# Optimization experiments

Measured on AMD Instinct MI355X. Metric: run time of the kernel, lower is better.

The kernel has to match this reference:

```python
import jax, jax.numpy as jnp
import numpy as np

B, T, D = 4, 2048, 2048
H, HD = 16, 128          # heads, head_dim (H*HD == D)
I = 5632                 # intermediate size
CAP = 0.25
K = int(T * CAP)         # 512 tokens selected per batch row
S = B * K                # packed sequence length
THETA = 10000.0
EPS = 1e-6


def setup_inputs() -> dict:
    key = jax.random.key(0)
    ks = jax.random.split(key, 12)
    s = 0.02
    w = lambda k, shp: jax.random.normal(k, shp, jnp.float32) * s
    return {
        "hidden_states": jax.random.normal(ks[0], (B, T, D), jnp.float32),
        "router_w": w(ks[1], (D,)),
        "router_b": jnp.zeros((1,), jnp.float32),
        "ln1_w": jnp.ones((D,), jnp.float32),
        "ln2_w": jnp.ones((D,), jnp.float32),
        "wq": w(ks[2], (D, D)), "bq": jnp.zeros((D,), jnp.float32),
        "wk": w(ks[3], (D, D)), "bk": jnp.zeros((D,), jnp.float32),
        "wv": w(ks[4], (D, D)), "bv": jnp.zeros((D,), jnp.float32),
        "wo": w(ks[5], (D, D)),
        "w_gate": w(ks[6], (D, I)),
        "w_up": w(ks[7], (D, I)),
        "w_down": w(ks[8], (I, D)),
    }


def _rms(x, w):
    return x * jax.lax.rsqrt(jnp.mean(x * x, axis=-1, keepdims=True) + EPS) * w


def _rotate_half(x):
    x1, x2 = jnp.split(x, 2, axis=-1)
    return jnp.concatenate([-x2, x1], axis=-1)


def reference(hidden_states, router_w, router_b, ln1_w, ln2_w,
              wq, bq, wk, bk, wv, bv, wo, w_gate, w_up, w_down):
    # ---- router: per-token scalar scores, top-k per batch row ----
    scores = hidden_states @ router_w + router_b[0]          # [B,T]
    _, idx = jax.lax.top_k(scores, K)                        # [B,K]
    idx = jnp.sort(idx, axis=-1)                             # causal order in packed seq

    # ---- gather selected tokens into packed batch-1 sequence ----
    sel = jnp.take_along_axis(hidden_states, idx[..., None], axis=1)  # [B,K,D]
    sel_scores = jnp.take_along_axis(scores, idx, axis=1)             # [B,K]
    x = sel.reshape(S, D)
    pos = idx.reshape(S)                                     # original token positions

    # ---- rotary tables gathered at original positions ----
    inv_freq = 1.0 / (THETA ** (jnp.arange(0, HD, 2, dtype=jnp.float32) / HD))
    freqs = pos.astype(jnp.float32)[:, None] * inv_freq[None, :]      # [S,HD/2]
    emb = jnp.concatenate([freqs, freqs], axis=-1)                    # [S,HD]
    cos, sin = jnp.cos(emb)[:, None, :], jnp.sin(emb)[:, None, :]     # [S,1,HD]

    # ---- Qwen2 decoder block (attention) ----
    h = _rms(x, ln1_w)
    q = (h @ wq + bq).reshape(S, H, HD)
    k = (h @ wk + bk).reshape(S, H, HD)
    v = (h @ wv + bv).reshape(S, H, HD)
    q = q * cos + _rotate_half(q) * sin
    k = k * cos + _rotate_half(k) * sin

    att = jnp.einsum("shd,thd->hst", q, k) / np.sqrt(HD).astype(np.float32)
    causal = jnp.tril(jnp.ones((S, S), bool))
    att = jnp.where(causal[None], att, jnp.finfo(att.dtype).min)
    p = jax.nn.softmax(att, axis=-1)
    attn_out = jnp.einsum("hst,thd->shd", p, v).reshape(S, D) @ wo
    x1 = x + attn_out

    # ---- Qwen2 decoder block (SwiGLU MLP) ----
    h2 = _rms(x1, ln2_w)
    mlp = (jax.nn.silu(h2 @ w_gate) * (h2 @ w_up)) @ w_down
    processed = x1 + mlp                                     # [S,D]

    # ---- sigmoid gate blend + scatter back ----
    gate = jax.nn.sigmoid(sel_scores).reshape(S, 1)
    blended = gate * processed + (1.0 - gate) * x            # [S,D]
    out = hidden_states.at[jnp.arange(B)[:, None], idx].set(blended.reshape(B, K, D))
    return out
```

## Files before the change

kernel.cpp:

```cpp
#include <hip/hip_runtime.h>
#include <stdint.h>

#define B_ 4
#define T_ 2048
#define D_ 2048
#define H_ 16
#define HD_ 128
#define I_ 5632
#define K_ 512
#define S_ 2048
#define D3_ (3 * D_)

typedef float f32x4 __attribute__((ext_vector_type(4)));
typedef short s16x8 __attribute__((ext_vector_type(8)));
typedef __bf16 bf16x8 __attribute__((ext_vector_type(8)));

template <typename V>
__device__ __forceinline__ auto mfma_try(V a, V b, f32x4 c, int)
    -> decltype(__builtin_amdgcn_mfma_f32_16x16x32_bf16(a, b, c, 0, 0, 0)) {
  return __builtin_amdgcn_mfma_f32_16x16x32_bf16(a, b, c, 0, 0, 0);
}
template <typename V>
__device__ __forceinline__ f32x4 mfma_try(V a, V b, f32x4 c, long) {
  return __builtin_amdgcn_mfma_f32_16x16x32_bf16(
      __builtin_bit_cast(bf16x8, a), __builtin_bit_cast(bf16x8, b), c, 0, 0, 0);
}
__device__ __forceinline__ f32x4 mfma_bf16(s16x8 a, s16x8 b, f32x4 c) {
  return mfma_try(a, b, c, 0);
}

__device__ __forceinline__ void gl_lds16(const void* g, void* l) {
  __builtin_amdgcn_global_load_lds((const __attribute__((address_space(1))) void*)g,
                                   (__attribute__((address_space(3))) void*)l, 16, 0, 0);
}

__device__ __forceinline__ unsigned short f2bf(float f) {
  unsigned u = __float_as_uint(f);
  u += 0x7FFFu + ((u >> 16) & 1);
  return (unsigned short)(u >> 16);
}
__device__ __forceinline__ float bf2f(unsigned short s) {
  return __uint_as_float(((unsigned)s) << 16);
}

__global__ __launch_bounds__(256) void k_copy_scores(const float4* __restrict__ hid,
                                                     float4* __restrict__ dst,
                                                     const float4* __restrict__ rw,
                                                     const float* __restrict__ rb,
                                                     float* __restrict__ scores) {
  int row = blockIdx.x, t = threadIdx.x;
  const float4* hr = hid + (size_t)row * (D_ / 4);
  float4* dr = dst + (size_t)row * (D_ / 4);
  float acc = 0.f;
#pragma unroll
  for (int i = 0; i < 2; i++) {
    float4 v = hr[t + i * 256];
    dr[t + i * 256] = v;
    float4 w = rw[t + i * 256];
    acc += v.x * w.x + v.y * w.y + v.z * w.z + v.w * w.w;
  }
#pragma unroll
  for (int d = 32; d; d >>= 1) acc += __shfl_xor(acc, d);
  __shared__ float red[4];
  if ((t & 63) == 0) red[t >> 6] = acc;
  __syncthreads();
  if (t == 0) scores[row] = red[0] + red[1] + red[2] + red[3] + rb[0];
}

__global__ __launch_bounds__(1024) void k_topk(const float* __restrict__ scores,
                                               int* __restrict__ pos) {
  __shared__ unsigned long long keys[T_];
  __shared__ int sidx[K_];
  int b = blockIdx.x, t = threadIdx.x;
  for (int i = t; i < T_; i += 1024) {
    unsigned u = __float_as_uint(scores[b * T_ + i]);
    u = (u & 0x80000000u) ? ~u : (u | 0x80000000u);
    keys[i] = ((unsigned long long)u << 32) | (unsigned)(~(unsigned)i);
  }
  __syncthreads();
  for (int k = 2; k <= T_; k <<= 1)
    for (int j = k >> 1; j > 0; j >>= 1) {
      for (int i = t; i < T_; i += 1024) {
        int l = i ^ j;
        if (l > i) {
          unsigned long long a = keys[i], c = keys[l];
          bool desc = ((i & k) == 0);
          if (desc ? (a < c) : (a > c)) { keys[i] = c; keys[l] = a; }
        }
      }
      __syncthreads();
    }
  if (t < K_) sidx[t] = (int)(~(unsigned)(keys[t] & 0xFFFFFFFFull));
  __syncthreads();
  for (int k = 2; k <= K_; k <<= 1)
    for (int j = k >> 1; j > 0; j >>= 1) {
      if (t < K_) {
        int i = t, l = i ^ j;
        if (l > i && l < K_) {
          int a = sidx[i], c = sidx[l];
          bool asc = ((i & k) == 0);
          if (asc ? (a > c) : (a < c)) { sidx[i] = c; sidx[l] = a; }
        }
      }
      __syncthreads();
    }
  if (t < K_) pos[b * K_ + t] = sidx[t];
}

__global__ __launch_bounds__(256) void k_gather(const float* __restrict__ hidden,
    const int* __restrict__ pos, const float* __restrict__ scores,
    const float* __restrict__ ln1w, float* __restrict__ x,
    unsigned short* __restrict__ xn, float* __restrict__ gate,
    float* __restrict__ cosb, float* __restrict__ sinb) {
  int s = blockIdx.x, t = threadIdx.x;
  int b = s >> 9, p = pos[s];
  const float* src = hidden + ((size_t)b * T_ + p) * D_;
  float v[8];
  float ss = 0.f;
#pragma unroll
  for (int i = 0; i < 8; i++) { v[i] = src[t + i * 256]; ss += v[i] * v[i]; }
  __shared__ float red[4];
#pragma unroll
  for (int d = 32; d; d >>= 1) ss += __shfl_xor(ss, d);
  if ((t & 63) == 0) red[t >> 6] = ss;
  __syncthreads();
  ss = red[0] + red[1] + red[2] + red[3];
  float scale = rsqrtf(ss / (float)D_ + 1e-6f);
  float* xd = x + (size_t)s * D_;
  unsigned short* xnd = xn + (size_t)s * D_;
#pragma unroll
  for (int i = 0; i < 8; i++) {
    int c = t + i * 256;
    xd[c] = v[i];
    xnd[c] = f2bf(v[i] * scale * ln1w[c]);
  }
  if (t == 0) gate[s] = 1.f / (1.f + expf(-scores[b * T_ + p]));
  if (t < 64) {
    float invf = powf(10000.0f, -(float)t / 64.0f);
    float f = (float)p * invf;
    cosb[s * 64 + t] = cosf(f);
    sinb[s * 64 + t] = sinf(f);
  }
}

__global__ __launch_bounds__(256) void k_transpose(const float* __restrict__ src,
                                                   unsigned short* __restrict__ dst,
                                                   int R, int C) {
  __shared__ float tile[32][33];
  int tx = threadIdx.x & 31, ty = threadIdx.x >> 5;
  int c0 = blockIdx.x * 32, r0 = blockIdx.y * 32;
#pragma unroll
  for (int i = 0; i < 4; i++) {
    int r = ty + i * 8;
    tile[r][tx] = src[(size_t)(r0 + r) * C + c0 + tx];
  }
  __syncthreads();
  int drow = threadIdx.x >> 3;
  int dc4 = (threadIdx.x & 7) * 4;
  ushort4 v;
  v.x = f2bf(tile[dc4 + 0][drow]);
  v.y = f2bf(tile[dc4 + 1][drow]);
  v.z = f2bf(tile[dc4 + 2][drow]);
  v.w = f2bf(tile[dc4 + 3][drow]);
  *(ushort4*)&dst[(size_t)(c0 + drow) * R + r0 + dc4] = v;
}

#define SWZ(row) ((((row) >> 1) & 3) << 4)

__device__ __forceinline__ void stage16k(const unsigned short* __restrict__ g, int ldK,
                                         int row0, int k0, char* lds, int tid) {
#pragma unroll
  for (int c = 0; c < 2; c++) {
    int off = c * 8192 + tid * 16;
    int row = off >> 6;
    int cb = (off & 63) ^ SWZ(row);
    gl_lds16(g + (size_t)(row0 + row) * ldK + k0 + (cb >> 1), lds + off);
  }
}
__device__ __forceinline__ void stage8k(const unsigned short* __restrict__ g, int ldK,
                                        int row0, int k0, char* lds, int tid) {
  int off = tid * 16;
  int row = off >> 6;
  int cb = (off & 63) ^ SWZ(row);
  gl_lds16(g + (size_t)(row0 + row) * ldK + k0 + (cb >> 1), lds + off);
}
__device__ __forceinline__ void stage64r(const unsigned short* __restrict__ g, int ldK,
                                         int row0, int k0, char* lds, int tid) {
  int off = tid * 16;
  int row = off >> 6;
  int cb = (off & 63) ^ SWZ(row);
  gl_lds16(g + (size_t)(row0 + row) * ldK + k0 + (cb >> 1), lds + off);
}
__device__ __forceinline__ void stage128r(const unsigned short* __restrict__ g, int ldK,
                                          int row0, int k0, char* lds, int tid) {
#pragma unroll
  for (int c = 0; c < 2; c++) {
    int off = c * 4096 + tid * 16;
    int row = off >> 6;
    int cb = (off & 63) ^ SWZ(row);
    gl_lds16(g + (size_t)(row0 + row) * ldK + k0 + (cb >> 1), lds + off);
  }
}
__device__ __forceinline__ s16x8 ldfrag(const char* base, int row, int g) {
  return *(const s16x8*)(base + row * 64 + ((g * 16) ^ SWZ(row)));
}

__global__ __launch_bounds__(512, 2) void k_gemm_qkv8(const unsigned short* __restrict__ A,
    const unsigned short* __restrict__ Bt, unsigned short* __restrict__ C,
    const float* __restrict__ bq, const float* __restrict__ bk,
    const float* __restrict__ bv) {
  alignas(16) __shared__ short As[2][256 * 32];
  alignas(16) __shared__ short Bs[2][128 * 32];
  int tid = threadIdx.x;
  int lane = tid & 63, g = lane >> 4, lr = lane & 15;
  int wid = tid >> 6, wm = wid >> 1, wn = wid & 1;
  int m0 = blockIdx.x * 256, n0 = blockIdx.y * 128;
  f32x4 zero4 = {0.f, 0.f, 0.f, 0.f};
  f32x4 acc[4][4];
#pragma unroll
  for (int m = 0; m < 4; m++)
#pragma unroll
    for (int n = 0; n < 4; n++) acc[m][n] = zero4;
  const int nkt = D_ / 32;
  stage16k(A, D_, m0, 0, (char*)As[0], tid);
  stage8k(Bt, D_, n0, 0, (char*)Bs[0], tid);
  stage16k(A, D_, m0, 32, (char*)As[1], tid);
  stage8k(Bt, D_, n0, 32, (char*)Bs[1], tid);
  int arow = wm * 64 + lr;
  int brow = wn * 64 + lr;
  for (int t = 0; t < nkt; t++) {
    int b = t & 1;
    const char* Ab = (const char*)As[b];
    const char* Bb = (const char*)Bs[b];
    if (t + 1 < nkt) asm volatile("s_waitcnt vmcnt(3)" ::: "memory");
    else             asm volatile("s_waitcnt vmcnt(0)" ::: "memory");
    __builtin_amdgcn_s_barrier();
    s16x8 af[4], bf4[4];
#pragma unroll
    for (int i = 0; i < 4; i++) af[i] = ldfrag(Ab, arow + i * 16, g);
#pragma unroll
    for (int i = 0; i < 4; i++) bf4[i] = ldfrag(Bb, brow + i * 16, g);
    asm volatile("s_waitcnt lgkmcnt(0)" ::: "memory");
    __builtin_amdgcn_s_barrier();
    if (t + 2 < nkt) {
      stage16k(A, D_, m0, (t + 2) * 32, (char*)As[b], tid);
      stage8k(Bt, D_, n0, (t + 2) * 32, (char*)Bs[b], tid);
    }
    __builtin_amdgcn_s_setprio(1);
#pragma unroll
    for (int m = 0; m < 4; m++)
#pragma unroll
      for (int n = 0; n < 4; n++) acc[m][n] = mfma_bf16(af[m], bf4[n], acc[m][n]);
    __builtin_amdgcn_s_setprio(0);
  }
#pragma unroll
  for (int m = 0; m < 4; m++)
#pragma unroll
    for (int n = 0; n < 4; n++)
#pragma unroll
      for (int r = 0; r < 4; r++) {
        int row = m0 + wm * 64 + m * 16 + (g << 2) + r;
        int col = n0 + wn * 64 + n * 16 + lr;
        float bias = (col < D_) ? bq[col] : ((col < 2 * D_) ? bk[col - D_] : bv[col - 2 * D_]);
        C[(size_t)row * D3_ + col] = f2bf(acc[m][n][r] + bias);
      }
}

__device__ __forceinline__ void stage_u(const unsigned short* __restrict__ g, int ldK,
                                        int grow0, int k0, char* ldsbase, int tid) {
#pragma unroll
  for (int c = 0; c < 2; c++) {
    int off = c * 8192 + tid * 16;
    int row = off >> 7;
    int cb = (off & 127) ^ ((row & 7) << 4);
    gl_lds16(g + (size_t)(grow0 + row) * ldK + k0 + (cb >> 1), ldsbase + off);
  }
}
__device__ __forceinline__ s16x8 ldfrag128(const char* base, int row, int byteoff) {
  return *(const s16x8*)(base + row * 128 + (byteoff ^ ((row & 7) << 4)));
}

#define GUP_MFMA(AF, BB, ACC)                                       \
  __builtin_amdgcn_s_barrier();                                     \
  asm volatile("s_waitcnt lgkmcnt(0)" ::: "memory");                \
  __builtin_amdgcn_sched_barrier(0);                                \
  __builtin_amdgcn_s_setprio(1);                                    \
  _Pragma("unroll") for (int m = 0; m < 4; m++)                     \
    _Pragma("unroll") for (int n = 0; n < 4; n++)                   \
      ACC[m][n] = mfma_bf16(AF[m], BB[n], ACC[m][n]);               \
  __builtin_amdgcn_s_setprio(0);                                    \
  __builtin_amdgcn_s_barrier();

__global__ __launch_bounds__(512, 1) void k_gemm_gup8p(const unsigned short* __restrict__ A,
    const unsigned short* __restrict__ Bg, const unsigned short* __restrict__ Bu,
    unsigned short* __restrict__ act) {
  alignas(16) __shared__ char L[2][65536];
  int tid = threadIdx.x;
  int lane = tid & 63, g = lane >> 4, lr = lane & 15;
  int wid = tid >> 6, wm = wid >> 1, wn = wid & 1;
  int m0 = blockIdx.x * 256, n0 = blockIdx.y * 128;
  f32x4 zero4 = {0.f, 0.f, 0.f, 0.f};
  f32x4 ag[4][4], au[4][4];
#pragma unroll
  for (int m = 0; m < 4; m++)
#pragma unroll
    for (int n = 0; n < 4; n++) { ag[m][n] = zero4; au[m][n] = zero4; }
  int arow = wm * 64 + lr;
  int brow = wn * 64 + lr;
  const int NI = D_ / 128;
  stage_u(A, D_, m0, 0, &L[0][0], tid);
  stage_u(A, D_, m0 + 128, 0, &L[0][16384], tid);
  stage_u(Bg, D_, n0, 0, &L[0][32768], tid);
  stage_u(Bu, D_, n0, 0, &L[0][49152], tid);
  stage_u(A, D_, m0, 64, &L[1][0], tid);
  asm volatile("s_waitcnt vmcnt(2)" ::: "memory");
  __builtin_amdgcn_s_barrier();
  for (int i = 0; i < NI; i++) {
    const char* B0 = &L[0][0];
    const char* B1 = &L[1][0];
    int k1 = i * 128 + 64;
    int k2 = i * 128 + 128;
    int k3 = i * 128 + 192;
    bool more = (i + 1 < NI);
    s16x8 af0[4], af1[4], bb[4];
#pragma unroll
    for (int q = 0; q < 4; q++) af0[q] = ldfrag128(B0, arow + q * 16, g * 16);
#pragma unroll
    for (int q = 0; q < 4; q++) bb[q] = ldfrag128(B0 + 32768, brow + q * 16, g * 16);
    stage_u(A, D_, m0 + 128, k1, &L[1][16384], tid);
    asm volatile("s_waitcnt vmcnt(4)" ::: "memory");
    GUP_MFMA(af0, bb, ag);
#pragma unroll
    for (int q = 0; q < 4; q++) bb[q] = ldfrag128(B0 + 49152, brow + q * 16, g * 16);
    stage_u(Bg, D_, n0, k1, &L[1][32768], tid);
    GUP_MFMA(af0, bb, au);
#pragma unroll
    for (int q = 0; q < 4; q++) af1[q] = ldfrag128(B0, arow + q * 16, 64 + g * 16);
#pragma unroll
    for (int q = 0; q < 4; q++) bb[q] = ldfrag128(B0 + 32768, brow + q * 16, 64 + g * 16);
    stage_u(Bu, D_, n0, k1, &L[1][49152], tid);
    GUP_MFMA(af1, bb, ag);
#pragma unroll
    for (int q = 0; q < 4; q++) bb[q] = ldfrag128(B0 + 49152, brow + q * 16, 64 + g * 16);
    if (more) {
      stage_u(A, D_, m0, k2, &L[0][0], tid);
      asm volatile("s_waitcnt vmcnt(4)" ::: "memory");
    } else {
      asm volatile("s_waitcnt vmcnt(0)" ::: "memory");
    }
    GUP_MFMA(af1, bb, au);
#pragma unroll
    for (int q = 0; q < 4; q++) af0[q] = ldfrag128(B1, arow + q * 16, g * 16);
#pragma unroll
    for (int q = 0; q < 4; q++) bb[q] = ldfrag128(B1 + 32768, brow + q * 16, g * 16);
    if (more) stage_u(A, D_, m0 + 128, k2, &L[0][16384], tid);
    asm volatile("s_waitcnt vmcnt(4)" ::: "memory");
    GUP_MFMA(af0, bb, ag);
#pragma unroll
    for (int q = 0; q < 4; q++) bb[q] = ldfrag128(B1 + 49152, brow + q * 16, g * 16);
    if (more) stage_u(Bg, D_, n0, k2, &L[0][32768], tid);
    GUP_MFMA(af0, bb, au);
#pragma unroll
    for (int q = 0; q < 4; q++) af1[q] = ldfrag128(B1, arow + q * 16, 64 + g * 16);
#pragma unroll
    for (int q = 0; q < 4; q++) bb[q] = ldfrag128(B1 + 32768, brow + q * 16, 64 + g * 16);
    if (more) stage_u(Bu, D_, n0, k2, &L[0][49152], tid);
    GUP_MFMA(af1, bb, ag);
#pragma unroll
    for (int q = 0; q < 4; q++) bb[q] = ldfrag128(B1 + 49152, brow + q * 16, 64 + g * 16);
    if (more) stage_u(A, D_, m0, k3, &L[1][0], tid);
    asm volatile("s_waitcnt vmcnt(4)" ::: "memory");
    GUP_MFMA(af1, bb, au);
  }
#pragma unroll
  for (int m = 0; m < 4; m++)
#pragma unroll
    for (int n = 0; n < 4; n++)
#pragma unroll
      for (int r = 0; r < 4; r++) {
        int row = m0 + wm * 64 + m * 16 + (g << 2) + r;
        int col = n0 + wn * 64 + n * 16 + lr;
        float gv = ag[m][n][r], uv = au[m][n][r];
        float si = gv / (1.f + __expf(-gv));
        act[(size_t)row * I_ + col] = f2bf(si * uv);
      }
}

__global__ __launch_bounds__(256, 2) void k_gemm_wo64(const unsigned short* __restrict__ A,
    const unsigned short* __restrict__ Bt, const float* __restrict__ xres,
    float* __restrict__ x1) {
  alignas(16) __shared__ short As[2][64 * 32];
  alignas(16) __shared__ short Bs[2][128 * 32];
  int tid = threadIdx.x;
  int lane = tid & 63, g = lane >> 4, lr = lane & 15, wid = tid >> 6;
  int m0 = blockIdx.x * 64, n0 = blockIdx.y * 128;
  f32x4 zero4 = {0.f, 0.f, 0.f, 0.f};
  f32x4 acc[4][2];
#pragma unroll
  for (int m = 0; m < 4; m++)
#pragma unroll
    for (int n = 0; n < 2; n++) acc[m][n] = zero4;
  const int nkt = D_ / 32;
  stage64r(A, D_, m0, 0, (char*)As[0], tid);
  stage128r(Bt, D_, n0, 0, (char*)Bs[0], tid);
  stage64r(A, D_, m0, 32, (char*)As[1], tid);
  stage128r(Bt, D_, n0, 32, (char*)Bs[1], tid);
  for (int t = 0; t < nkt; t++) {
    int b = t & 1;
    const char* Ab = (const char*)As[b];
    const char* Bb = (const char*)Bs[b];
    if (t + 1 < nkt) asm volatile("s_waitcnt vmcnt(3)" ::: "memory");
    else             asm volatile("s_waitcnt vmcnt(0)" ::: "memory");
    __builtin_amdgcn_s_barrier();
    s16x8 af[4], bf2[2];
#pragma unroll
    for (int i = 0; i < 4; i++) af[i] = ldfrag(Ab, i * 16 + lr, g);
#pragma unroll
    for (int j = 0; j < 2; j++) bf2[j] = ldfrag(Bb, wid * 32 + j * 16 + lr, g);
    asm volatile("s_waitcnt lgkmcnt(0)" ::: "memory");
    __builtin_amdgcn_s_barrier();
    if (t + 2 < nkt) {
      stage64r(A, D_, m0, (t + 2) * 32, (char*)As[b], tid);
      stage128r(Bt, D_, n0, (t + 2) * 32, (char*)Bs[b], tid);
    }
    __builtin_amdgcn_s_setprio(1);
#pragma unroll
    for (int m = 0; m < 4; m++)
#pragma unroll
      for (int n = 0; n < 2; n++) acc[m][n] = mfma_bf16(af[m], bf2[n], acc[m][n]);
    __builtin_amdgcn_s_setprio(0);
  }
#pragma unroll
  for (int m = 0; m < 4; m++)
#pragma unroll
    for (int n = 0; n < 2; n++)
#pragma unroll
      for (int r = 0; r < 4; r++) {
        int row = m0 + m * 16 + (g << 2) + r;
        int col = n0 + wid * 32 + n * 16 + lr;
        x1[(size_t)row * D_ + col] = acc[m][n][r] + xres[(size_t)row * D_ + col];
      }
}

__global__ __launch_bounds__(256, 2) void k_gemm_down64(const unsigned short* __restrict__ A,
    const unsigned short* __restrict__ Bt, const float* __restrict__ x1,
    const float* __restrict__ x, const float* __restrict__ gate,
    const int* __restrict__ pos, float* __restrict__ out) {
  alignas(16) __shared__ short As[2][64 * 32];
  alignas(16) __shared__ short Bs[2][128 * 32];
  int tid = threadIdx.x;
  int lane = tid & 63, g = lane >> 4, lr = lane & 15, wid = tid >> 6;
  int m0 = blockIdx.x * 64, n0 = blockIdx.y * 128;
  f32x4 zero4 = {0.f, 0.f, 0.f, 0.f};
  f32x4 acc[4][2];
#pragma unroll
  for (int m = 0; m < 4; m++)
#pragma unroll
    for (int n = 0; n < 2; n++) acc[m][n] = zero4;
  const int nkt = I_ / 32;
  stage64r(A, I_, m0, 0, (char*)As[0], tid);
  stage128r(Bt, I_, n0, 0, (char*)Bs[0], tid);
  stage64r(A, I_, m0, 32, (char*)As[1], tid);
  stage128r(Bt, I_, n0, 32, (char*)Bs[1], tid);
  for (int t = 0; t < nkt; t++) {
    int b = t & 1;
    const char* Ab = (const char*)As[b];
    const char* Bb = (const char*)Bs[b];
    if (t + 1 < nkt) asm volatile("s_waitcnt vmcnt(3)" ::: "memory");
    else             asm volatile("s_waitcnt vmcnt(0)" ::: "memory");
    __builtin_amdgcn_s_barrier();
    s16x8 af[4], bf2[2];
#pragma unroll
    for (int i = 0; i < 4; i++) af[i] = ldfrag(Ab, i * 16 + lr, g);
#pragma unroll
    for (int j = 0; j < 2; j++) bf2[j] = ldfrag(Bb, wid * 32 + j * 16 + lr, g);
    asm volatile("s_waitcnt lgkmcnt(0)" ::: "memory");
    __builtin_amdgcn_s_barrier();
    if (t + 2 < nkt) {
      stage64r(A, I_, m0, (t + 2) * 32, (char*)As[b], tid);
      stage128r(Bt, I_, n0, (t + 2) * 32, (char*)Bs[b], tid);
    }
    __builtin_amdgcn_s_setprio(1);
#pragma unroll
    for (int m = 0; m < 4; m++)
#pragma unroll
      for (int n = 0; n < 2; n++) acc[m][n] = mfma_bf16(af[m], bf2[n], acc[m][n]);
    __builtin_amdgcn_s_setprio(0);
  }
#pragma unroll
  for (int m = 0; m < 4; m++)
#pragma unroll
    for (int n = 0; n < 2; n++)
#pragma unroll
      for (int r = 0; r < 4; r++) {
        int srow = m0 + m * 16 + (g << 2) + r;
        int col = n0 + wid * 32 + n * 16 + lr;
        float proc = acc[m][n][r] + x1[(size_t)srow * D_ + col];
        float gt = gate[srow];
        float xv = x[(size_t)srow * D_ + col];
        int bb = srow >> 9;
        int p = pos[srow];
        out[((size_t)bb * T_ + p) * D_ + col] = gt * proc + (1.f - gt) * xv;
      }
}

__global__ __launch_bounds__(256) void k_rope(const unsigned short* __restrict__ qkv,
    const float* __restrict__ cosb, const float* __restrict__ sinb,
    unsigned short* __restrict__ qh, unsigned short* __restrict__ kh,
    unsigned short* __restrict__ vT) {
  int s0 = blockIdx.x * 64;
  int h = blockIdx.y;
  int t = threadIdx.x;
#pragma unroll
  for (int i = 0; i < 16; i++) {
    int flat = t + i * 256;
    int r = flat >> 6, dp = flat & 63;
    int s = s0 + r;
    float c = cosb[s * 64 + dp], sn = sinb[s * 64 + dp];
    const unsigned short* qrow = qkv + (size_t)s * D3_ + h * HD_;
    float q1 = bf2f(qrow[dp]), q2 = bf2f(qrow[dp + 64]);
    unsigned short* qdst = qh + ((size_t)h * S_ + s) * HD_;
    qdst[dp] = f2bf(q1 * c - q2 * sn);
    qdst[dp + 64] = f2bf(q2 * c + q1 * sn);
    const unsigned short* krow = qrow + D_;
    float k1 = bf2f(krow[dp]), k2 = bf2f(krow[dp + 64]);
    unsigned short* kdst = kh + ((size_t)h * S_ + s) * HD_;
    kdst[dp] = f2bf(k1 * c - k2 * sn);
    kdst[dp + 64] = f2bf(k2 * c + k1 * sn);
  }
  __shared__ unsigned short vt[128][66];
#pragma unroll
  for (int i = 0; i < 32; i++) {
    int flat = t + i * 256;
    int r = flat >> 7, d = flat & 127;
    vt[d][r] = qkv[(size_t)(s0 + r) * D3_ + 2 * D_ + h * HD_ + d];
  }
  __syncthreads();
#pragma unroll
  for (int i = 0; i < 32; i++) {
    int flat = t + i * 256;
    int d = flat >> 6, sc = flat & 63;
    vT[((size_t)h * HD_ + d) * S_ + s0 + sc] = vt[d][sc];
  }
}

__device__ __forceinline__ void stage_kv(const unsigned short* __restrict__ kh,
                                         const unsigned short* __restrict__ vT,
                                         size_t hbase, int kt, char* KsB, char* VsB, int tid) {
#pragma unroll
  for (int c = 0; c < 4; c++) {
    int off = c * 4096 + tid * 16;
    int row = off >> 8;
    int cb = (off & 255) ^ ((row & 7) << 4);
    gl_lds16(kh + hbase + (size_t)(kt * 64 + row) * HD_ + (cb >> 1), KsB + off);
  }
#pragma unroll
  for (int c = 0; c < 4; c++) {
    int off = c * 4096 + tid * 16;
    int row = off >> 7;
    int cb = (off & 127) ^ ((row & 7) << 4);
    gl_lds16(vT + hbase + (size_t)row * S_ + kt * 64 + (cb >> 1), VsB + off);
  }
}

__global__ __launch_bounds__(256, 2) void k_attn(const unsigned short* __restrict__ qh,
                                                 const unsigned short* __restrict__ kh,
                                                 const unsigned short* __restrict__ vT,
                                                 unsigned short* __restrict__ ao) {
  alignas(16) __shared__ short Ks[2][64 * 128];
  alignas(16) __shared__ short Vs[2][128 * 64];
  alignas(16) __shared__ short Ps[4][16 * 64];
  int bidx = blockIdx.x;
  int head = bidx & 15;
  int slot = bidx >> 4;
  int qt = (slot < 16) ? (31 - slot) : (slot - 16);
  int q0 = qt * 64;
  int tid = threadIdx.x, w = tid >> 6, lane = tid & 63, g = lane >> 4, lr = lane & 15;
  size_t hbase = (size_t)head * S_ * HD_;
  int qw = q0 + w * 16;
  char* PsW = (char*)&Ps[w][0];
  s16x8 qf[4];
#pragma unroll
  for (int ks = 0; ks < 4; ks++)
    qf[ks] = *(const s16x8*)&qh[hbase + (size_t)(qw + lr) * HD_ + ks * 32 + g * 8];
  f32x4 o[8];
  f32x4 zero4 = {0.f, 0.f, 0.f, 0.f};
#pragma unroll
  for (int nf = 0; nf < 8; nf++) o[nf] = zero4;
  float m_i[4], l_i[4];
#pragma unroll
  for (int r = 0; r < 4; r++) { m_i[r] = -1e30f; l_i[r] = 0.f; }
  const float sc = 0.08838834764831843f;

  stage_kv(kh, vT, hbase, 0, (char*)Ks[0], (char*)Vs[0], tid);
  if (qt > 0) stage_kv(kh, vT, hbase, 1, (char*)Ks[1], (char*)Vs[1], tid);

  for (int kt = 0; kt <= qt; kt++) {
    int b = kt & 1;
    const char* KsB = (const char*)Ks[b];
    const char* VsB = (const char*)Vs[b];
    if (kt < qt) asm volatile("s_waitcnt vmcnt(8)" ::: "memory");
    else         asm volatile("s_waitcnt vmcnt(0)" ::: "memory");
    __builtin_amdgcn_s_barrier();
    f32x4 sacc[4];
#pragma unroll
    for (int nf = 0; nf < 4; nf++) sacc[nf] = zero4;
#pragma unroll
    for (int ks = 0; ks < 4; ks++) {
      s16x8 kf[4];
#pragma unroll
      for (int nf = 0; nf < 4; nf++) {
        int row = nf * 16 + lr;
        kf[nf] = *(const s16x8*)(KsB + row * 256 + (((ks << 6) + (g << 4)) ^ ((row & 7) << 4)));
      }
#pragma unroll
      for (int nf = 0; nf < 4; nf++) sacc[nf] = mfma_bf16(qf[ks], kf[nf], sacc[nf]);
    }
    bool diag = (kt == qt);
#pragma unroll
    for (int r = 0; r < 4; r++) {
      int prow = (g << 2) + r;
      int qrow = qw + prow;
      float pv[4];
      float mx = -1e30f;
#pragma unroll
      for (int nf = 0; nf < 4; nf++) {
        float vv = sacc[nf][r] * sc;
        if (diag) {
          int kc = kt * 64 + nf * 16 + lr;
          vv = (kc <= qrow) ? vv : -1e30f;
        }
        pv[nf] = vv;
        mx = fmaxf(mx, vv);
      }
#pragma unroll
      for (int d = 1; d < 16; d <<= 1) mx = fmaxf(mx, __shfl_xor(mx, d));
      float mold = m_i[r], mnew = fmaxf(mold, mx);
      float corr = __expf(mold - mnew);
      float ssum = 0.f;
#pragma unroll
      for (int nf = 0; nf < 4; nf++) {
        float pe = __expf(pv[nf] - mnew);
        int cb = ((nf * 16 + lr) << 1) ^ ((prow & 7) << 4);
        *(unsigned short*)(PsW + prow * 128 + cb) = f2bf(pe);
        ssum += pe;
      }
#pragma unroll
      for (int d = 1; d < 16; d <<= 1) ssum += __shfl_xor(ssum, d);
      l_i[r] = l_i[r] * corr + ssum;
      m_i[r] = mnew;
#pragma unroll
      for (int nf = 0; nf < 8; nf++) o[nf][r] *= corr;
    }
    s16x8 pa[2];
#pragma unroll
    for (int ks = 0; ks < 2; ks++)
      pa[ks] = *(const s16x8*)(PsW + lr * 128 + (((ks << 6) + (g << 4)) ^ ((lr & 7) << 4)));
#pragma unroll
    for (int nf = 0; nf < 8; nf++) {
#pragma unroll
      for (int ks = 0; ks < 2; ks++) {
        int row = nf * 16 + lr;
        s16x8 vb = *(const s16x8*)(VsB + row * 128 + (((ks << 6) + (g << 4)) ^ ((row & 7) << 4)));
        o[nf] = mfma_bf16(pa[ks], vb, o[nf]);
      }
    }
    asm volatile("s_waitcnt lgkmcnt(0)" ::: "memory");
    __builtin_amdgcn_s_barrier();
    if (kt + 2 <= qt)
      stage_kv(kh, vT, hbase, kt + 2, (char*)Ks[b], (char*)Vs[b], tid);
  }
#pragma unroll
  for (int nf = 0; nf < 8; nf++)
#pragma unroll
    for (int r = 0; r < 4; r++) {
      int row = qw + (g << 2) + r;
      int col = head * HD_ + nf * 16 + lr;
      ao[(size_t)row * D_ + col] = f2bf(o[nf][r] / l_i[r]);
    }
}

__global__ __launch_bounds__(256) void k_rms2(const float* __restrict__ x1,
                                              const float* __restrict__ ln2w,
                                              unsigned short* __restrict__ xn2) {
  int s = blockIdx.x, t = threadIdx.x;
  const float* src = x1 + (size_t)s * D_;
  float v[8];
  float ss = 0.f;
#pragma unroll
  for (int i = 0; i < 8; i++) { v[i] = src[t + i * 256]; ss += v[i] * v[i]; }
  __shared__ float red[4];
#pragma unroll
  for (int d = 32; d; d >>= 1) ss += __shfl_xor(ss, d);
  if ((t & 63) == 0) red[t >> 6] = ss;
  __syncthreads();
  ss = red[0] + red[1] + red[2] + red[3];
  float scale = rsqrtf(ss / (float)D_ + 1e-6f);
  unsigned short* dst = xn2 + (size_t)s * D_;
#pragma unroll
  for (int i = 0; i < 8; i++) {
    int c = t + i * 256;
    dst[c] = f2bf(v[i] * scale * ln2w[c]);
  }
}

extern "C" void kernel_launch(void* const* d_in, const int* in_sizes, int n_in,
                              void* d_out, int out_size, void* d_ws, size_t ws_size,
                              hipStream_t stream) {
  (void)in_sizes; (void)n_in; (void)out_size; (void)ws_size;
  const float* hidden = (const float*)d_in[0];
  const float* router_w = (const float*)d_in[1];
  const float* router_b = (const float*)d_in[2];
  const float* ln1w = (const float*)d_in[3];
  const float* ln2w = (const float*)d_in[4];
  const float* wq = (const float*)d_in[5];
  const float* bq = (const float*)d_in[6];
  const float* wk = (const float*)d_in[7];
  const float* bk = (const float*)d_in[8];
  const float* wv = (const float*)d_in[9];
  const float* bv = (const float*)d_in[10];
  const float* wo = (const float*)d_in[11];
  const float* wg = (const float*)d_in[12];
  const float* wu = (const float*)d_in[13];
  const float* wd = (const float*)d_in[14];
  float* out = (float*)d_out;

  char* ws = (char*)d_ws;
  size_t off = 0;
  auto alloc = [&](size_t bytes) {
    char* p = ws + off;
    off += (bytes + 255) & ~(size_t)255;
    return p;
  };
  unsigned short* wqkvT = (unsigned short*)alloc(3ull * D_ * D_ * 2);
  unsigned short* woT = (unsigned short*)alloc((size_t)D_ * D_ * 2);
  unsigned short* wgT = (unsigned short*)alloc((size_t)I_ * D_ * 2);
  unsigned short* wuT = (unsigned short*)alloc((size_t)I_ * D_ * 2);
  unsigned short* wdT = (unsigned short*)alloc((size_t)D_ * I_ * 2);
  float* scores = (float*)alloc((size_t)B_ * T_ * 4);
  int* pos = (int*)alloc((size_t)S_ * 4);
  float* gate = (float*)alloc((size_t)S_ * 4);
  float* x = (float*)alloc((size_t)S_ * D_ * 4);
  float* x1 = (float*)alloc((size_t)S_ * D_ * 4);
  unsigned short* xn = (unsigned short*)alloc((size_t)S_ * D_ * 2);
  float* cosb = (float*)alloc((size_t)S_ * 64 * 4);
  float* sinb = (float*)alloc((size_t)S_ * 64 * 4);
  unsigned short* qkv = (unsigned short*)alloc((size_t)S_ * D3_ * 2);
  unsigned short* qh = (unsigned short*)alloc((size_t)H_ * S_ * HD_ * 2);
  unsigned short* kh = (unsigned short*)alloc((size_t)H_ * S_ * HD_ * 2);
  unsigned short* vT = (unsigned short*)alloc((size_t)H_ * S_ * HD_ * 2);
  unsigned short* ao = (unsigned short*)alloc((size_t)S_ * D_ * 2);

  k_copy_scores<<<B_ * T_, 256, 0, stream>>>((const float4*)hidden, (float4*)out,
                                             (const float4*)router_w, router_b, scores);

  k_transpose<<<dim3(D_ / 32, D_ / 32), 256, 0, stream>>>(wq, wqkvT, D_, D_);
  k_transpose<<<dim3(D_ / 32, D_ / 32), 256, 0, stream>>>(wk, wqkvT + (size_t)D_ * D_, D_, D_);
  k_transpose<<<dim3(D_ / 32, D_ / 32), 256, 0, stream>>>(wv, wqkvT + 2ull * D_ * D_, D_, D_);
  k_transpose<<<dim3(D_ / 32, D_ / 32), 256, 0, stream>>>(wo, woT, D_, D_);
  k_transpose<<<dim3(I_ / 32, D_ / 32), 256, 0, stream>>>(wg, wgT, D_, I_);
  k_transpose<<<dim3(I_ / 32, D_ / 32), 256, 0, stream>>>(wu, wuT, D_, I_);
  k_transpose<<<dim3(D_ / 32, I_ / 32), 256, 0, stream>>>(wd, wdT, I_, D_);

  k_topk<<<B_, 1024, 0, stream>>>(scores, pos);
  k_gather<<<S_, 256, 0, stream>>>(hidden, pos, scores, ln1w, x, xn, gate, cosb, sinb);

  k_gemm_qkv8<<<dim3(S_ / 256, D3_ / 128), 512, 0, stream>>>(xn, wqkvT, qkv, bq, bk, bv);
  k_rope<<<dim3(S_ / 64, H_), 256, 0, stream>>>(qkv, cosb, sinb, qh, kh, vT);
  k_attn<<<32 * H_, 256, 0, stream>>>(qh, kh, vT, ao);
  k_gemm_wo64<<<dim3(S_ / 64, D_ / 128), 256, 0, stream>>>(ao, woT, x, x1);
  k_rms2<<<S_, 256, 0, stream>>>(x1, ln2w, xn);
  k_gemm_gup8p<<<dim3(S_ / 256, I_ / 128), 512, 0, stream>>>(xn, wgT, wuT, qkv);
  k_gemm_down64<<<dim3(S_ / 64, D_ / 128), 256, 0, stream>>>(qkv, wdT, x1, x, gate, pos, out);
}
```

Baseline: 537.5 us.

## Use 256x256 ping-pong QKV GEMM and batch weight transposes into fewer launches

Replaces the 256x128 double-buffered QKV GEMM with a 256x256 tile kernel using 128-wide K stages, a 64KB-per-buffer LDS ping-pong and phased MFMA blocks interleaved with async global-to-LDS loads, modeled on the gate/up kernel. The larger tile raises arithmetic intensity per byte loaded, and the phased schedule aims to overlap loads with compute. The trade-off is one block per CU, fewer blocks (192), and more accumulator registers. Separately, the weight transposes are merged into two batched launches via blockIdx.z to cut launch overhead.

```diff
diff --git a/kernel.cpp b/kernel.cpp
--- a/kernel.cpp
+++ b/kernel.cpp
@@ -143,9 +143,9 @@
   }
 }
 
-__global__ __launch_bounds__(256) void k_transpose(const float* __restrict__ src,
-                                                   unsigned short* __restrict__ dst,
-                                                   int R, int C) {
+__device__ __forceinline__ void transpose_body(const float* __restrict__ src,
+                                               unsigned short* __restrict__ dst,
+                                               int R, int C) {
   __shared__ float tile[32][33];
   int tx = threadIdx.x & 31, ty = threadIdx.x >> 5;
   int c0 = blockIdx.x * 32, r0 = blockIdx.y * 32;
@@ -164,26 +164,30 @@
   v.w = f2bf(tile[dc4 + 3][drow]);
   *(ushort4*)&dst[(size_t)(c0 + drow) * R + r0 + dc4] = v;
 }
+__global__ __launch_bounds__(256) void k_transpose(const float* __restrict__ src,
+                                                   unsigned short* __restrict__ dst,
+                                                   int R, int C) {
+  transpose_body(src, dst, R, C);
+}
+__global__ __launch_bounds__(256) void k_transpose4(const float* s0, const float* s1,
+                                                    const float* s2, const float* s3,
+                                                    unsigned short* d0, unsigned short* d1,
+                                                    unsigned short* d2, unsigned short* d3,
+                                                    int R, int C) {
+  int z = blockIdx.z;
+  const float* src = (z == 0) ? s0 : (z == 1) ? s1 : (z == 2) ? s2 : s3;
+  unsigned short* dst = (z == 0) ? d0 : (z == 1) ? d1 : (z == 2) ? d2 : d3;
+  transpose_body(src, dst, R, C);
+}
+__global__ __launch_bounds__(256) void k_transpose2(const float* s0, const float* s1,
+                                                    unsigned short* d0, unsigned short* d1,
+                                                    int R, int C) {
+  int z = blockIdx.z;
+  transpose_body(z ? s1 : s0, z ? d1 : d0, R, C);
+}
 
 #define SWZ(row) ((((row) >> 1) & 3) << 4)
 
-__device__ __forceinline__ void stage16k(const unsigned short* __restrict__ g, int ldK,
-                                         int row0, int k0, char* lds, int tid) {
-#pragma unroll
-  for (int c = 0; c < 2; c++) {
-    int off = c * 8192 + tid * 16;
-    int row = off >> 6;
-    int cb = (off & 63) ^ SWZ(row);
-    gl_lds16(g + (size_t)(row0 + row) * ldK + k0 + (cb >> 1), lds + off);
-  }
-}
-__device__ __forceinline__ void stage8k(const unsigned short* __restrict__ g, int ldK,
-                                        int row0, int k0, char* lds, int tid) {
-  int off = tid * 16;
-  int row = off >> 6;
-  int cb = (off & 63) ^ SWZ(row);
-  gl_lds16(g + (size_t)(row0 + row) * ldK + k0 + (cb >> 1), lds + off);
-}
 __device__ __forceinline__ void stage64r(const unsigned short* __restrict__ g, int ldK,
                                          int row0, int k0, char* lds, int tid) {
   int off = tid * 16;
@@ -205,67 +209,6 @@
   return *(const s16x8*)(base + row * 64 + ((g * 16) ^ SWZ(row)));
 }
 
-__global__ __launch_bounds__(512, 2) void k_gemm_qkv8(const unsigned short* __restrict__ A,
-    const unsigned short* __restrict__ Bt, unsigned short* __restrict__ C,
-    const float* __restrict__ bq, const float* __restrict__ bk,
-    const float* __restrict__ bv) {
-  alignas(16) __shared__ short As[2][256 * 32];
-  alignas(16) __shared__ short Bs[2][128 * 32];
-  int tid = threadIdx.x;
-  int lane = tid & 63, g = lane >> 4, lr = lane & 15;
-  int wid = tid >> 6, wm = wid >> 1, wn = wid & 1;
-  int m0 = blockIdx.x * 256, n0 = blockIdx.y * 128;
-  f32x4 zero4 = {0.f, 0.f, 0.f, 0.f};
-  f32x4 acc[4][4];
-#pragma unroll
-  for (int m = 0; m < 4; m++)
-#pragma unroll
-    for (int n = 0; n < 4; n++) acc[m][n] = zero4;
-  const int nkt = D_ / 32;
-  stage16k(A, D_, m0, 0, (char*)As[0], tid);
-  stage8k(Bt, D_, n0, 0, (char*)Bs[0], tid);
-  stage16k(A, D_, m0, 32, (char*)As[1], tid);
-  stage8k(Bt, D_, n0, 32, (char*)Bs[1], tid);
-  int arow = wm * 64 + lr;
-  int brow = wn * 64 + lr;
-  for (int t = 0; t < nkt; t++) {
-    int b = t & 1;
-    const char* Ab = (const char*)As[b];
-    const char* Bb = (const char*)Bs[b];
-    if (t + 1 < nkt) asm volatile("s_waitcnt vmcnt(3)" ::: "memory");
-    else             asm volatile("s_waitcnt vmcnt(0)" ::: "memory");
-    __builtin_amdgcn_s_barrier();
-    s16x8 af[4], bf4[4];
-#pragma unroll
-    for (int i = 0; i < 4; i++) af[i] = ldfrag(Ab, arow + i * 16, g);
-#pragma unroll
-    for (int i = 0; i < 4; i++) bf4[i] = ldfrag(Bb, brow + i * 16, g);
-    asm volatile("s_waitcnt lgkmcnt(0)" ::: "memory");
-    __builtin_amdgcn_s_barrier();
-    if (t + 2 < nkt) {
-      stage16k(A, D_, m0, (t + 2) * 32, (char*)As[b], tid);
-      stage8k(Bt, D_, n0, (t + 2) * 32, (char*)Bs[b], tid);
-    }
-    __builtin_amdgcn_s_setprio(1);
-#pragma unroll
-    for (int m = 0; m < 4; m++)
-#pragma unroll
-      for (int n = 0; n < 4; n++) acc[m][n] = mfma_bf16(af[m], bf4[n], acc[m][n]);
-    __builtin_amdgcn_s_setprio(0);
-  }
-#pragma unroll
-  for (int m = 0; m < 4; m++)
-#pragma unroll
-    for (int n = 0; n < 4; n++)
-#pragma unroll
-      for (int r = 0; r < 4; r++) {
-        int row = m0 + wm * 64 + m * 16 + (g << 2) + r;
-        int col = n0 + wn * 64 + n * 16 + lr;
-        float bias = (col < D_) ? bq[col] : ((col < 2 * D_) ? bk[col - D_] : bv[col - 2 * D_]);
-        C[(size_t)row * D3_ + col] = f2bf(acc[m][n][r] + bias);
-      }
-}
-
 __device__ __forceinline__ void stage_u(const unsigned short* __restrict__ g, int ldK,
                                         int grow0, int k0, char* ldsbase, int tid) {
 #pragma unroll
@@ -280,7 +223,7 @@
   return *(const s16x8*)(base + row * 128 + (byteoff ^ ((row & 7) << 4)));
 }
 
-#define GUP_MFMA(AF, BB, ACC)                                       \
+#define PHASE_MFMA(AF, BB, ACC)                                     \
   __builtin_amdgcn_s_barrier();                                     \
   asm volatile("s_waitcnt lgkmcnt(0)" ::: "memory");                \
   __builtin_amdgcn_sched_barrier(0);                                \
@@ -290,6 +233,93 @@
       ACC[m][n] = mfma_bf16(AF[m], BB[n], ACC[m][n]);               \
   __builtin_amdgcn_s_setprio(0);                                    \
   __builtin_amdgcn_s_barrier();
+
+__global__ __launch_bounds__(512, 1) void k_gemm_qkv8p(const unsigned short* __restrict__ A,
+    const unsigned short* __restrict__ Bt, unsigned short* __restrict__ C,
+    const float* __restrict__ bq, const float* __restrict__ bk,
+    const float* __restrict__ bv) {
+  alignas(16) __shared__ char L[2][65536];
+  int tid = threadIdx.x;
+  int lane = tid & 63, g = lane >> 4, lr = lane & 15;
+  int wid = tid >> 6, wm = wid >> 2, wn = wid & 3;
+  int m0 = blockIdx.x * 256, n0 = blockIdx.y * 256;
+  f32x4 zero4 = {0.f, 0.f, 0.f, 0.f};
+  f32x4 acc[8][4];
+#pragma unroll
+  for (int m = 0; m < 8; m++)
+#pragma unroll
+    for (int n = 0; n < 4; n++) acc[m][n] = zero4;
+  f32x4(*accLo)[4] = &acc[0];
+  f32x4(*accHi)[4] = &acc[4];
+  int arow = wm * 128 + lr;
+  int brow = wn * 64 + lr;
+  const int NI = D_ / 128;
+  stage_u(A, D_, m0, 0, &L[0][0], tid);
+  stage_u(A, D_, m0 + 128, 0, &L[0][16384], tid);
+  stage_u(Bt, D_, n0, 0, &L[0][32768], tid);
+  stage_u(Bt, D_, n0 + 128, 0, &L[0][49152], tid);
+  stage_u(A, D_, m0, 64, &L[1][0], tid);
+  asm volatile("s_waitcnt vmcnt(2)" ::: "memory");
+  __builtin_amdgcn_s_barrier();
+  for (int i = 0; i < NI; i++) {
+    const char* Buf0 = &L[0][0];
+    const char* Buf1 = &L[1][0];
+    int k1 = i * 128 + 64, k2 = i * 128 + 128, k3 = i * 128 + 192;
+    bool more = (i + 1 < NI);
+    s16x8 af[8], bf[4];
+#pragma unroll
+    for (int q = 0; q < 8; q++) af[q] = ldfrag128(Buf0, arow + q * 16, g * 16);
+#pragma unroll
+    for (int q = 0; q < 4; q++) bf[q] = ldfrag128(Buf0 + 32768, brow + q * 16, g * 16);
+    stage_u(A, D_, m0 + 128, k1, &L[1][16384], tid);
+    PHASE_MFMA(af, bf, accLo);
+    stage_u(Bt, D_, n0, k1, &L[1][32768], tid);
+    PHASE_MFMA((af + 4), bf, accHi);
+#pragma unroll
+    for (int q = 0; q < 8; q++) af[q] = ldfrag128(Buf0, arow + q * 16, 64 + g * 16);
+#pragma unroll
+    for (int q = 0; q < 4; q++) bf[q] = ldfrag128(Buf0 + 32768, brow + q * 16, 64 + g * 16);
+    stage_u(Bt, D_, n0 + 128, k1, &L[1][49152], tid);
+    PHASE_MFMA(af, bf, accLo);
+    if (more) {
+      stage_u(A, D_, m0, k2, &L[0][0], tid);
+      asm volatile("s_waitcnt vmcnt(2)" ::: "memory");
+    } else {
+      asm volatile("s_waitcnt vmcnt(0)" ::: "memory");
+    }
+    PHASE_MFMA((af + 4), bf, accHi);
+#pragma unroll
+    for (int q = 0; q < 8; q++) af[q] = ldfrag128(Buf1, arow + q * 16, g * 16);
+#pragma unroll
+    for (int q = 0; q < 4; q++) bf[q] = ldfrag128(Buf1 + 32768, brow + q * 16, g * 16);
+    if (more) stage_u(A, D_, m0 + 128, k2, &L[0][16384], tid);
+    PHASE_MFMA(af, bf, accLo);
+    if (more) stage_u(Bt, D_, n0, k2, &L[0][32768], tid);
+    PHASE_MFMA((af + 4), bf, accHi);
+#pragma unroll
+    for (int q = 0; q < 8; q++) af[q] = ldfrag128(Buf1, arow + q * 16, 64 + g * 16);
+#pragma unroll
+    for (int q = 0; q < 4; q++) bf[q] = ldfrag128(Buf1 + 32768, brow + q * 16, 64 + g * 16);
+    if (more) stage_u(Bt, D_, n0 + 128, k2, &L[0][49152], tid);
+    PHASE_MFMA(af, bf, accLo);
+    if (more) {
+      stage_u(A, D_, m0, k3, &L[1][0], tid);
+      asm volatile("s_waitcnt vmcnt(2)" ::: "memory");
+    }
+    PHASE_MFMA((af + 4), bf, accHi);
+  }
+#pragma unroll
+  for (int m = 0; m < 8; m++)
+#pragma unroll
+    for (int n = 0; n < 4; n++)
+#pragma unroll
+      for (int r = 0; r < 4; r++) {
+        int row = m0 + wm * 128 + m * 16 + (g << 2) + r;
+        int col = n0 + wn * 64 + n * 16 + lr;
+        float bias = (col < D_) ? bq[col] : ((col < 2 * D_) ? bk[col - D_] : bv[col - 2 * D_]);
+        C[(size_t)row * D3_ + col] = f2bf(acc[m][n][r] + bias);
+      }
+}
 
 __global__ __launch_bounds__(512, 1) void k_gemm_gup8p(const unsigned short* __restrict__ A,
     const unsigned short* __restrict__ Bg, const unsigned short* __restrict__ Bu,
@@ -329,17 +359,17 @@
     for (int q = 0; q < 4; q++) bb[q] = ldfrag128(B0 + 32768, brow + q * 16, g * 16);
     stage_u(A, D_, m0 + 128, k1, &L[1][16384], tid);
     asm volatile("s_waitcnt vmcnt(4)" ::: "memory");
-    GUP_MFMA(af0, bb, ag);
+    PHASE_MFMA(af0, bb, ag);
 #pragma unroll
     for (int q = 0; q < 4; q++) bb[q] = ldfrag128(B0 + 49152, brow + q * 16, g * 16);
     stage_u(Bg, D_, n0, k1, &L[1][32768], tid);
-    GUP_MFMA(af0, bb, au);
+    PHASE_MFMA(af0, bb, au);
 #pragma unroll
     for (int q = 0; q < 4; q++) af1[q] = ldfrag128(B0, arow + q * 16, 64 + g * 16);
 #pragma unroll
     for (int q = 0; q < 4; q++) bb[q] = ldfrag128(B0 + 32768, brow + q * 16, 64 + g * 16);
     stage_u(Bu, D_, n0, k1, &L[1][49152], tid);
-    GUP_MFMA(af1, bb, ag);
+    PHASE_MFMA(af1, bb, ag);
 #pragma unroll
     for (int q = 0; q < 4; q++) bb[q] = ldfrag128(B0 + 49152, brow + q * 16, 64 + g * 16);
     if (more) {
@@ -348,29 +378,29 @@
     } else {
       asm volatile("s_waitcnt vmcnt(0)" ::: "memory");
     }
-    GUP_MFMA(af1, bb, au);
+    PHASE_MFMA(af1, bb, au);
 #pragma unroll
     for (int q = 0; q < 4; q++) af0[q] = ldfrag128(B1, arow + q * 16, g * 16);
 #pragma unroll
     for (int q = 0; q < 4; q++) bb[q] = ldfrag128(B1 + 32768, brow + q * 16, g * 16);
     if (more) stage_u(A, D_, m0 + 128, k2, &L[0][16384], tid);
     asm volatile("s_waitcnt vmcnt(4)" ::: "memory");
-    GUP_MFMA(af0, bb, ag);
+    PHASE_MFMA(af0, bb, ag);
 #pragma unroll
     for (int q = 0; q < 4; q++) bb[q] = ldfrag128(B1 + 49152, brow + q * 16, g * 16);
     if (more) stage_u(Bg, D_, n0, k2, &L[0][32768], tid);
-    GUP_MFMA(af0, bb, au);
+    PHASE_MFMA(af0, bb, au);
 #pragma unroll
     for (int q = 0; q < 4; q++) af1[q] = ldfrag128(B1, arow + q * 16, 64 + g * 16);
 #pragma unroll
     for (int q = 0; q < 4; q++) bb[q] = ldfrag128(B1 + 32768, brow + q * 16, 64 + g * 16);
     if (more) stage_u(Bu, D_, n0, k2, &L[0][49152], tid);
-    GUP_MFMA(af1, bb, ag);
+    PHASE_MFMA(af1, bb, ag);
 #pragma unroll
     for (int q = 0; q < 4; q++) bb[q] = ldfrag128(B1 + 49152, brow + q * 16, 64 + g * 16);
     if (more) stage_u(A, D_, m0, k3, &L[1][0], tid);
     asm volatile("s_waitcnt vmcnt(4)" ::: "memory");
-    GUP_MFMA(af1, bb, au);
+    PHASE_MFMA(af1, bb, au);
   }
 #pragma unroll
   for (int m = 0; m < 4; m++)
@@ -754,18 +784,15 @@
   k_copy_scores<<<B_ * T_, 256, 0, stream>>>((const float4*)hidden, (float4*)out,
                                              (const float4*)router_w, router_b, scores);
 
-  k_transpose<<<dim3(D_ / 32, D_ / 32), 256, 0, stream>>>(wq, wqkvT, D_, D_);
-  k_transpose<<<dim3(D_ / 32, D_ / 32), 256, 0, stream>>>(wk, wqkvT + (size_t)D_ * D_, D_, D_);
-  k_transpose<<<dim3(D_ / 32, D_ / 32), 256, 0, stream>>>(wv, wqkvT + 2ull * D_ * D_, D_, D_);
-  k_transpose<<<dim3(D_ / 32, D_ / 32), 256, 0, stream>>>(wo, woT, D_, D_);
-  k_transpose<<<dim3(I_ / 32, D_ / 32), 256, 0, stream>>>(wg, wgT, D_, I_);
-  k_transpose<<<dim3(I_ / 32, D_ / 32), 256, 0, stream>>>(wu, wuT, D_, I_);
+  k_transpose4<<<dim3(D_ / 32, D_ / 32, 4), 256, 0, stream>>>(
+      wq, wk, wv, wo, wqkvT, wqkvT + (size_t)D_ * D_, wqkvT + 2ull * D_ * D_, woT, D_, D_);
+  k_transpose2<<<dim3(I_ / 32, D_ / 32, 2), 256, 0, stream>>>(wg, wu, wgT, wuT, D_, I_);
   k_transpose<<<dim3(D_ / 32, I_ / 32), 256, 0, stream>>>(wd, wdT, I_, D_);
 
   k_topk<<<B_, 1024, 0, stream>>>(scores, pos);
   k_gather<<<S_, 256, 0, stream>>>(hidden, pos, scores, ln1w, x, xn, gate, cosb, sinb);
 
-  k_gemm_qkv8<<<dim3(S_ / 256, D3_ / 128), 512, 0, stream>>>(xn, wqkvT, qkv, bq, bk, bv);
+  k_gemm_qkv8p<<<dim3(S_ / 256, D3_ / 256), 512, 0, stream>>>(xn, wqkvT, qkv, bq, bk, bv);
   k_rope<<<dim3(S_ / 64, H_), 256, 0, stream>>>(qkv, cosb, sinb, qh, kh, vT);
   k_attn<<<32 * H_, 256, 0, stream>>>(qh, kh, vT, ao);
   k_gemm_wo64<<<dim3(S_ / 64, D_ / 128), 256, 0, stream>>>(ao, woT, x, x1);
```

Result: faster. 523.5 us (-2.6%).
